# Kernel optimization log

Measured on AMD Instinct MI355X. Metric: run time of the kernel, lower is better.

Reference implementation:

```python
import jax, jax.numpy as jnp
import numpy as np

N = 50000   # nodes
E = 800000  # edges
R = 8       # relations
B = 4       # bases
NEG = 0.2   # leaky relu slope


def setup_inputs() -> dict:
    key = jax.random.key(0)
    ks = jax.random.split(key, 20)
    s = 0.1
    rn = lambda k, sh: jax.random.normal(k, sh, dtype=jnp.float32) * s
    return {
        "x": jax.random.normal(ks[0], (N, 64), dtype=jnp.float32),
        "edge_index": jax.random.randint(ks[1], (2, E), 0, N),
        "edge_type": jax.random.randint(ks[2], (E,), 0, R),
        # RGCN layer 1 (64 -> 64), basis decomposition
        "basis1": rn(ks[3], (B, 64, 64)), "comp1": rn(ks[4], (R, B)),
        "root1": rn(ks[5], (64, 64)), "brg1": jnp.zeros((64,), jnp.float32),
        # GAT layer 1 (64 -> 32, heads=4, concat -> 128)
        "wg1": rn(ks[6], (64, 128)), "asrc1": rn(ks[7], (4, 32)),
        "adst1": rn(ks[8], (4, 32)), "bg1": jnp.zeros((128,), jnp.float32),
        # RGCN layer 2 (128 -> 32)
        "basis2": rn(ks[9], (B, 128, 32)), "comp2": rn(ks[10], (R, B)),
        "root2": rn(ks[11], (128, 32)), "brg2": jnp.zeros((32,), jnp.float32),
        # GAT layer 2 (32 -> 16, heads=4, concat=False -> mean)
        "wg2": rn(ks[12], (32, 64)), "asrc2": rn(ks[13], (4, 16)),
        "adst2": rn(ks[14], (4, 16)), "bg2": jnp.zeros((16,), jnp.float32),
    }


def rgcn(x, src, dst, etype, basis, comp, root, bias):
    """PyG RGCNConv with basis decomposition, aggr='mean' per relation."""
    n, f = x.shape
    weight = jnp.einsum('rb,bio->rio', comp, basis)          # [R, in, out]
    seg = dst * R + etype                                    # per (node, relation) segment
    msg = x[src]                                             # [E, in] gather
    sums = jax.ops.segment_sum(msg, seg, num_segments=n * R).reshape(n, R, f)
    cnt = jax.ops.segment_sum(jnp.ones((src.shape[0],), x.dtype), seg,
                              num_segments=n * R).reshape(n, R, 1)
    mean = sums / jnp.maximum(cnt, 1.0)                      # [N, R, in]
    return jnp.einsum('nri,rio->no', mean, weight) + x @ root + bias


def gat(x, src, dst, w, a_src, a_dst, bias, heads, out_ch, concat):
    """PyG GATConv: add self loops, edge softmax over incoming edges."""
    n = x.shape[0]
    loop = jnp.arange(n)
    s2 = jnp.concatenate([src, loop])
    d2 = jnp.concatenate([dst, loop])
    h = (x @ w).reshape(n, heads, out_ch)                    # [N, H, C]
    al_src = (h * a_src).sum(-1)                             # [N, H]
    al_dst = (h * a_dst).sum(-1)                             # [N, H]
    e = jax.nn.leaky_relu(al_src[s2] + al_dst[d2], NEG)      # [E2, H]
    m = jax.ops.segment_max(e, d2, num_segments=n)           # stable softmax per dst
    e = jnp.exp(e - m[d2])
    z = jax.ops.segment_sum(e, d2, num_segments=n)
    alpha = e / z[d2]                                        # [E2, H]
    msg = h[s2] * alpha[:, :, None]                          # [E2, H, C]
    out = jax.ops.segment_sum(msg, d2, num_segments=n)       # [N, H, C]
    out = out.reshape(n, heads * out_ch) if concat else out.mean(axis=1)
    return out + bias


def reference(x, edge_index, edge_type,
              basis1, comp1, root1, brg1, wg1, asrc1, adst1, bg1,
              basis2, comp2, root2, brg2, wg2, asrc2, adst2, bg2):
    src, dst = edge_index[0], edge_index[1]
    # i=0: RGCN + relu (dropout p=0)
    x = jax.nn.relu(rgcn(x, src, dst, edge_type, basis1, comp1, root1, brg1))
    # i=1 == 2*pairs-1: GAT concat, NO activation
    x = gat(x, src, dst, wg1, asrc1, adst1, bg1, heads=4, out_ch=32, concat=True)
    # i=2: RGCN + relu
    x = jax.nn.relu(rgcn(x, src, dst, edge_type, basis2, comp2, root2, brg2))
    # i=3: GAT mean-heads + relu
    x = jax.nn.relu(gat(x, src, dst, wg2, asrc2, adst2, bg2, heads=4, out_ch=16, concat=False))
    return jnp.tanh(x)
```

## Files before the change

### kernel.cpp

```cpp
#include <hip/hip_runtime.h>
#include <math.h>

#define NN 50000
#define EE 800000
#define RR 8
#define SLOPE 0.2f
#define SEGS (NN * RR)
#define NBLK ((SEGS + 255) / 256)
#define NTW ((NN + 63) / 64)
#define NBUK 98
#define SEGB 4096
#define EB4 ((EE + 4095) / 4096)

typedef __attribute__((ext_vector_type(8))) short bf16x8;
typedef __attribute__((ext_vector_type(4))) float f32x4;
typedef _Float16 f16;
typedef __attribute__((ext_vector_type(4))) _Float16 h4;
typedef __attribute__((ext_vector_type(8))) _Float16 h8;

__device__ __forceinline__ float leaky(float v) { return v >= 0.f ? v : SLOPE * v; }

__device__ __forceinline__ void fmacc(float4& a, const float4& v, float p) {
    a.x = fmaf(v.x, p, a.x);
    a.y = fmaf(v.y, p, a.y);
    a.z = fmaf(v.z, p, a.z);
    a.w = fmaf(v.w, p, a.w);
}

__device__ __forceinline__ void red4(float4& a, int m) {
    a.x += __shfl_xor(a.x, m);
    a.y += __shfl_xor(a.y, m);
    a.z += __shfl_xor(a.z, m);
    a.w += __shfl_xor(a.w, m);
}

__device__ __forceinline__ float4 h4tof4(h4 t) {
    return make_float4((float)t.x, (float)t.y, (float)t.z, (float)t.w);
}

__device__ __forceinline__ void split8(const float4& v0, const float4& v1,
                                       bf16x8& hi, bf16x8& lo) {
    float e[8] = {v0.x, v0.y, v0.z, v0.w, v1.x, v1.y, v1.z, v1.w};
    union { bf16x8 v; unsigned u[4]; } H, L;
#pragma unroll
    for (int j = 0; j < 4; j++) {
        unsigned b0 = __float_as_uint(e[2 * j]), b1 = __float_as_uint(e[2 * j + 1]);
        unsigned h0 = b0 & 0xFFFF0000u, h1 = b1 & 0xFFFF0000u;
        H.u[j] = (h0 >> 16) | h1;
        float l0 = e[2 * j] - __uint_as_float(h0);
        float l1 = e[2 * j + 1] - __uint_as_float(h1);
        L.u[j] = (__float_as_uint(l0) >> 16) | (__float_as_uint(l1) & 0xFFFF0000u);
    }
    hi = H.v;
    lo = L.v;
}

__global__ void k_count2(const int* __restrict__ dst, const int* __restrict__ et,
                         int* __restrict__ cnt2) {
    int e = blockIdx.x * 256 + threadIdx.x;
    if (e < EE) atomicAdd(&cnt2[dst[e] * RR + et[e]], 1);
}

__global__ void k_scanA(const int* __restrict__ cnt2, int* __restrict__ rp,
                        int* __restrict__ bsum) {
    __shared__ int sh[256];
    int t = threadIdx.x;
    int i = blockIdx.x * 256 + t;
    int v = (i < SEGS) ? cnt2[i] : 0;
    sh[t] = v;
    __syncthreads();
    for (int off = 1; off < 256; off <<= 1) {
        int u = (t >= off) ? sh[t - off] : 0;
        __syncthreads();
        sh[t] += u;
        __syncthreads();
    }
    if (i < SEGS) rp[i] = sh[t] - v;
    if (t == 255) bsum[blockIdx.x] = sh[255];
}

__global__ void k_scanB(int* __restrict__ bsum) {
    __shared__ int sh[256];
    int t = threadIdx.x;
    int loc[8];
    int s = 0;
#pragma unroll
    for (int i = 0; i < 8; i++) {
        int idx = t * 8 + i;
        int v = (idx < NBLK) ? bsum[idx] : 0;
        loc[i] = v;
        s += v;
    }
    sh[t] = s;
    __syncthreads();
    for (int off = 1; off < 256; off <<= 1) {
        int u = (t >= off) ? sh[t - off] : 0;
        __syncthreads();
        sh[t] += u;
        __syncthreads();
    }
    int run = sh[t] - s;
#pragma unroll
    for (int i = 0; i < 8; i++) {
        int idx = t * 8 + i;
        if (idx < NBLK) {
            int v = loc[i];
            bsum[idx] = run;
            run += v;
        }
    }
}

__global__ void k_scanC(int* __restrict__ rp, const int* __restrict__ bsum) {
    int i = blockIdx.x * 256 + threadIdx.x;
    if (i < SEGS) rp[i] += bsum[blockIdx.x];
    if (i == 0) rp[SEGS] = EE;
}

__global__ void k_initcb(const int* __restrict__ rp, int* __restrict__ cbcur) {
    int t = threadIdx.x;
    if (t < NBUK) cbcur[t] = rp[t * SEGB];
}

__global__ __launch_bounds__(256) void k_fillA(const int* __restrict__ src,
                                               const int* __restrict__ dst,
                                               const int* __restrict__ et,
                                               int* __restrict__ cbcur,
                                               int* __restrict__ recbuf) {
    __shared__ int hist[NBUK], lcur[NBUK], gres[NBUK];
    int tid = threadIdx.x;
    int e0 = blockIdx.x * 4096;
    int cnt = EE - e0;
    if (cnt > 4096) cnt = 4096;
    for (int i = tid; i < NBUK; i += 256) { hist[i] = 0; lcur[i] = 0; }
    __syncthreads();
    int myb[16], myrec[16];
#pragma unroll
    for (int j = 0; j < 16; j++) {
        int i = tid + j * 256;
        if (i < cnt) {
            int e = e0 + i;
            int d = dst[e];
            int b = d >> 9;
            myb[j] = b;
            myrec[j] = ((d & 511) << 19) | (src[e] << 3) | et[e];
            atomicAdd(&hist[b], 1);
        } else {
            myb[j] = -1;
            myrec[j] = 0;
        }
    }
    __syncthreads();
    if (tid < NBUK) gres[tid] = atomicAdd(&cbcur[tid], hist[tid]);
    __syncthreads();
#pragma unroll
    for (int j = 0; j < 16; j++) {
        if (myb[j] >= 0) {
            int p = atomicAdd(&lcur[myb[j]], 1);
            recbuf[gres[myb[j]] + p] = myrec[j];
        }
    }
}

__global__ __launch_bounds__(256) void k_fillB(const int* __restrict__ rp,
                                               const int* __restrict__ recbuf,
                                               int* __restrict__ srcs2) {
    __shared__ int cur[SEGB];
    int b = blockIdx.x;
    int segbase = b * SEGB;
    int nseg = SEGS - segbase;
    if (nseg > SEGB) nseg = SEGB;
    int base = rp[segbase];
    int tid = threadIdx.x;
    for (int s = tid; s < SEGB; s += 256)
        cur[s] = (s < nseg) ? (rp[segbase + s] - base) : 0;
    __syncthreads();
    int limit = rp[segbase + nseg];
    int cnt = limit - base;
    for (int i = tid; i < cnt; i += 256) {
        int rec = recbuf[base + i];
        int segl = ((rec >> 19) << 3) | (rec & 7);
        int p = atomicAdd(&cur[segl], 1);
        srcs2[base + p] = rec & 0x7FFFF;
    }
}

__global__ void k_prep(const float* __restrict__ wg1, const float* __restrict__ wg2,
                       const float* __restrict__ root1, const float* __restrict__ root2,
                       const float* __restrict__ basis1, const float* __restrict__ basis2,
                       const float* __restrict__ comp2,
                       const float* __restrict__ asrc1, const float* __restrict__ adst1,
                       const float* __restrict__ asrc2, const float* __restrict__ adst2,
                       float* __restrict__ Wcat2e, float* __restrict__ wg1r,
                       float* __restrict__ Wstk, float* __restrict__ U1p,
                       float* __restrict__ U2p, float* __restrict__ Wb1) {
    int idx = blockIdx.x * 256 + threadIdx.x;
    if (idx < 16384) {
        int h = idx >> 12, kc = idx & 4095;
        int k = kc >> 6, c = kc & 63;
        wg1r[idx] = (c < 32) ? wg1[k * 128 + h * 32 + c] : 0.f;
    } else if (idx < 24576) {
        int j = idx - 16384;
        int row = j >> 6, c = j & 63;
        int h = row >> 5, k = row & 31;
        Wstk[j] = (c < 16) ? wg2[k * 64 + h * 16 + c] : 0.f;
    } else if (idx < 32768) {
        int j = idx - 24576;
        int k = j >> 6, c = j & 63;
        Wcat2e[k * 320 + c] = (c < 32) ? root2[k * 32 + c] : 0.f;
    } else if (idx < 36864) {
        int j0 = idx - 32768;
        int k = j0 >> 6, j = j0 & 63;
        float s = 0.f;
        if (j < 8) {
            int h = j & 3;
            const float* a = (j < 4) ? asrc1 : adst1;
            for (int c = 0; c < 32; c++) s += wg1[k * 128 + h * 32 + c] * a[h * 32 + c];
        }
        U1p[j0] = s;
    } else if (idx < 38912) {
        int j0 = idx - 36864;
        int k = j0 >> 6, j = j0 & 63;
        float s = 0.f;
        if (j < 8) {
            int h = j & 3;
            const float* a = (j < 4) ? asrc2 : adst2;
            for (int c = 0; c < 16; c++) s += wg2[k * 64 + h * 16 + c] * a[h * 16 + c];
        }
        U2p[j0] = s;
    } else if (idx < 55296) {
        Wb1[idx - 38912] = basis1[idx - 38912];
    } else if (idx < 59392) {
        Wb1[idx - 38912] = root1[idx - 55296];
    } else if (idx < 92160) {
        int j = idx - 59392;
        int i = j >> 8, rc = j & 255;
        int r = rc >> 5, o = rc & 31;
        float acc = 0.f;
#pragma unroll
        for (int b = 0; b < 4; b++) acc += comp2[r * 4 + b] * basis2[b * 4096 + i * 32 + o];
        Wcat2e[i * 320 + 64 + rc] = acc;
    }
}

__global__ void k_pack(const float* __restrict__ Wb1, const float* __restrict__ wg1r,
                       const float* __restrict__ Wcat, short* __restrict__ pWb1,
                       short* __restrict__ pwg1r, short* __restrict__ pWcat) {
    int u = blockIdx.x * 256 + threadIdx.x;
    int lane = u & 63, pair = u >> 6;
    if (pair >= 136) return;
    int m = lane & 15, g = lane >> 4;
    const float* src;
    int ldB, col, k0;
    short* dst;
    if (pair < 40) {
        int ct = pair / 10, kc = pair % 10;
        src = Wb1; ldB = 64; col = ct * 16 + m; k0 = kc * 32 + g * 8;
        dst = pWb1 + pair * 1024 + lane * 8;
    } else if (pair < 56) {
        int q = pair - 40;
        int h = q >> 2, lp = q & 3, ct = lp >> 1, kc = lp & 1;
        src = wg1r + h * 4096; ldB = 64; col = ct * 16 + m; k0 = kc * 32 + g * 8;
        dst = pwg1r + q * 1024 + lane * 8;
    } else {
        int q = pair - 56;
        int p = q >> 4, lp = q & 15, ct = lp >> 2, kc = lp & 3;
        src = Wcat; ldB = 320; col = p * 64 + ct * 16 + m; k0 = kc * 32 + g * 8;
        dst = pWcat + q * 1024 + lane * 8;
    }
    float e[8];
#pragma unroll
    for (int r = 0; r < 8; r++) e[r] = src[(size_t)(k0 + r) * ldB + col];
    union { bf16x8 v; unsigned u4[4]; } H, L;
#pragma unroll
    for (int j = 0; j < 4; j++) {
        unsigned b0 = __float_as_uint(e[2 * j]), b1 = __float_as_uint(e[2 * j + 1]);
        unsigned h0 = b0 & 0xFFFF0000u, h1 = b1 & 0xFFFF0000u;
        H.u4[j] = (h0 >> 16) | h1;
        float l0 = e[2 * j] - __uint_as_float(h0);
        float l1 = e[2 * j + 1] - __uint_as_float(h1);
        L.u4[j] = (__float_as_uint(l0) >> 16) | (__float_as_uint(l1) & 0xFFFF0000u);
    }
    *(bf16x8*)dst = H.v;
    *(bf16x8*)(dst + 512) = L.v;
}

template <int KTOT, int NCOL, int ACT = 0, int OUTH = 0>
__global__ __launch_bounds__(256) void k_mfma(const float* __restrict__ X, int ldX, int xmb,
                                              const short* __restrict__ Bpk, int bmb,
                                              float* __restrict__ Y, int ldY, size_t ymb,
                                              const float* __restrict__ bias, int biasmb) {
    constexpr int NKC = KTOT / 32;
    constexpr int NCT = NCOL / 16;
    const int tid = threadIdx.x;
    const int wid = tid >> 6, lane = tid & 63;
    const int m = lane & 15, g = lane >> 4;
    const int mb = blockIdx.y;
    const int rowbase = blockIdx.x * 64 + wid * 16;
    if (rowbase >= NN) return;
    const float* Xm = X + (size_t)mb * xmb + (size_t)(rowbase + m) * ldX;
    const short* Bm = Bpk + (size_t)mb * bmb;

    f32x4 acc[NCT];
#pragma unroll
    for (int c = 0; c < NCT; c++) acc[c] = (f32x4){0.f, 0.f, 0.f, 0.f};

#pragma unroll
    for (int kc = 0; kc < NKC; kc++) {
        float4 v0 = *(const float4*)(Xm + kc * 32 + g * 8);
        float4 v1 = *(const float4*)(Xm + kc * 32 + g * 8 + 4);
        bf16x8 ah, al;
        split8(v0, v1, ah, al);
#pragma unroll
        for (int ct = 0; ct < NCT; ct++) {
            const short* bp = Bm + (size_t)(ct * NKC + kc) * 1024 + lane * 8;
            bf16x8 bh = *(const bf16x8*)bp;
            bf16x8 bl = *(const bf16x8*)(bp + 512);
            acc[ct] = __builtin_amdgcn_mfma_f32_16x16x32_bf16(ah, bh, acc[ct], 0, 0, 0);
            acc[ct] = __builtin_amdgcn_mfma_f32_16x16x32_bf16(al, bh, acc[ct], 0, 0, 0);
            acc[ct] = __builtin_amdgcn_mfma_f32_16x16x32_bf16(ah, bl, acc[ct], 0, 0, 0);
        }
    }

#pragma unroll
    for (int ct = 0; ct < NCT; ct++) {
        int col = ct * 16 + m;
        float bv = bias ? bias[mb * biasmb + col] : 0.f;
#pragma unroll
        for (int i = 0; i < 4; i++) {
            float o = acc[ct][i] + bv;
            if (ACT == 2) o = fmaxf(o, 0.f);
            if (OUTH) {
                f16* Yh = (f16*)Y;
                Yh[(size_t)mb * ymb + (size_t)(rowbase + g * 4 + i) * ldY + col] = (f16)o;
            } else {
                Y[(size_t)mb * ymb + (size_t)(rowbase + g * 4 + i) * ldY + col] = o;
            }
        }
    }
}

__global__ __launch_bounds__(256) void k_gagg1(const int* __restrict__ rp,
                                               const int* __restrict__ srcs2,
                                               const float* __restrict__ comp,
                                               const float* __restrict__ X,
                                               float* __restrict__ U) {
    __shared__ float4 sh_w[4][8];
    int wid = threadIdx.x >> 6, lane = threadIdx.x & 63;
    int n = blockIdx.x * 4 + wid;
    int rpv = (lane <= 8) ? rp[n * RR + lane] : 0;
    int nxt = __shfl(rpv, (lane + 1) & 63);
    if (lane < 8) {
        float inv = 1.f / (float)((nxt - rpv) > 0 ? (nxt - rpv) : 1);
        float4 c = *(const float4*)(comp + lane * 4);
        sh_w[wid][lane] = make_float4(c.x * inv, c.y * inv, c.z * inv, c.w * inv);
    }
    int q = lane & 15;
    int beg = rp[n * RR], end = rp[n * RR + RR];
    float4 a0 = make_float4(0.f, 0.f, 0.f, 0.f);
    float4 a1 = a0, a2 = a0, a3 = a0;
    int k = beg + (lane >> 4);
    for (; k + 4 < end; k += 8) {
        int key0 = srcs2[k], key1 = srcs2[k + 4];
        float4 w0 = sh_w[wid][key0 & 7], w1 = sh_w[wid][key1 & 7];
        float4 v0 = *(const float4*)(X + (size_t)(key0 >> 3) * 64 + q * 4);
        float4 v1 = *(const float4*)(X + (size_t)(key1 >> 3) * 64 + q * 4);
        fmacc(a0, v0, w0.x);
        fmacc(a1, v0, w0.y);
        fmacc(a2, v0, w0.z);
        fmacc(a3, v0, w0.w);
        fmacc(a0, v1, w1.x);
        fmacc(a1, v1, w1.y);
        fmacc(a2, v1, w1.z);
        fmacc(a3, v1, w1.w);
    }
    if (k < end) {
        int key0 = srcs2[k];
        float4 w0 = sh_w[wid][key0 & 7];
        float4 v0 = *(const float4*)(X + (size_t)(key0 >> 3) * 64 + q * 4);
        fmacc(a0, v0, w0.x);
        fmacc(a1, v0, w0.y);
        fmacc(a2, v0, w0.z);
        fmacc(a3, v0, w0.w);
    }
    red4(a0, 16); red4(a0, 32);
    red4(a1, 16); red4(a1, 32);
    red4(a2, 16); red4(a2, 32);
    red4(a3, 16); red4(a3, 32);
    if (lane < 16) {
        float* un = U + (size_t)n * 320;
        *(float4*)(un + 0 * 64 + q * 4) = a0;
        *(float4*)(un + 1 * 64 + q * 4) = a1;
        *(float4*)(un + 2 * 64 + q * 4) = a2;
        *(float4*)(un + 3 * 64 + q * 4) = a3;
        *(float4*)(un + 256 + q * 4) = *(const float4*)(X + (size_t)n * 64 + q * 4);
    }
}

__global__ __launch_bounds__(256) void k_alds1(const float* __restrict__ X,
                                               const float* __restrict__ U1p,
                                               float* __restrict__ alds,
                                               f16* __restrict__ x1h) {
    __shared__ float sUT[8 * 68];
    int tid = threadIdx.x;
    for (int i = tid; i < 512; i += 256) {
        int j = i >> 6, c = i & 63;
        sUT[j * 68 + c] = U1p[c * 64 + j];
    }
    __syncthreads();
    int lane = tid & 63, wid = tid >> 6;
    int n = blockIdx.x * 32 + wid * 8 + (lane >> 3);
    int q = lane & 7;
    float x[8];
    if (n < NN) {
        float4 v0 = *(const float4*)(X + (size_t)n * 64 + q * 8);
        float4 v1 = *(const float4*)(X + (size_t)n * 64 + q * 8 + 4);
        x[0] = v0.x; x[1] = v0.y; x[2] = v0.z; x[3] = v0.w;
        x[4] = v1.x; x[5] = v1.y; x[6] = v1.z; x[7] = v1.w;
        h8 hv;
#pragma unroll
        for (int c = 0; c < 8; c++) hv[c] = (f16)x[c];
        *(h8*)(x1h + (size_t)n * 64 + q * 8) = hv;
    } else {
#pragma unroll
        for (int c = 0; c < 8; c++) x[c] = 0.f;
    }
    float al[8];
#pragma unroll
    for (int j = 0; j < 8; j++) {
        const float* u = &sUT[j * 68 + q * 8];
        float s = 0.f;
#pragma unroll
        for (int c = 0; c < 8; c++) s += x[c] * u[c];
        al[j] = s;
    }
#pragma unroll
    for (int m = 1; m < 8; m <<= 1)
#pragma unroll
        for (int j = 0; j < 8; j++) al[j] += __shfl_xor(al[j], m);
    if (n < NN) alds[(size_t)n * 8 + q] = al[q];
}

__global__ __launch_bounds__(256) void k_final(const float* __restrict__ Xm,
                                               const float* __restrict__ Wstk,
                                               const float* __restrict__ bg2,
                                               float* __restrict__ out) {
    __shared__ float sWT[16 * 132];
    int tid = threadIdx.x;
    for (int i = tid; i < 2048; i += 256) {
        int c = i >> 7, k = i & 127;
        sWT[c * 132 + k] = Wstk[k * 64 + c];
    }
    __syncthreads();
    int lane = tid & 63, wid = tid >> 6;
    int n = blockIdx.x * 32 + wid * 8 + (lane >> 3);
    int q = lane & 7;
    float x[16];
    if (n < NN) {
#pragma unroll
        for (int t = 0; t < 4; t++) {
            float4 v = *(const float4*)(Xm + (size_t)n * 128 + t * 32 + q * 4);
            x[t * 4 + 0] = v.x; x[t * 4 + 1] = v.y; x[t * 4 + 2] = v.z; x[t * 4 + 3] = v.w;
        }
    } else {
#pragma unroll
        for (int k = 0; k < 16; k++) x[k] = 0.f;
    }
    float al[16];
#pragma unroll
    for (int c = 0; c < 16; c++) {
        float s = 0.f;
#pragma unroll
        for (int t = 0; t < 4; t++) {
            const float* w = &sWT[c * 132 + t * 32 + q * 4];
            s += x[t * 4 + 0] * w[0] + x[t * 4 + 1] * w[1] + x[t * 4 + 2] * w[2] +
                 x[t * 4 + 3] * w[3];
        }
        al[c] = s;
    }
#pragma unroll
    for (int m = 1; m < 8; m <<= 1)
#pragma unroll
        for (int c = 0; c < 16; c++) al[c] += __shfl_xor(al[c], m);
    if (n < NN && q < 4) {
        float4 bv = *(const float4*)(bg2 + q * 4);
        float4 v;
        v.x = tanhf(fmaxf(0.25f * al[q * 4 + 0] + bv.x, 0.f));
        v.y = tanhf(fmaxf(0.25f * al[q * 4 + 1] + bv.y, 0.f));
        v.z = tanhf(fmaxf(0.25f * al[q * 4 + 2] + bv.z, 0.f));
        v.w = tanhf(fmaxf(0.25f * al[q * 4 + 3] + bv.w, 0.f));
        *(float4*)(out + (size_t)n * 16 + q * 4) = v;
    }
}

__global__ __launch_bounds__(256) void k_agg2(const int* __restrict__ rp,
                                              const int* __restrict__ srcs2,
                                              const f16* __restrict__ y,
                                              const float* __restrict__ bias,
                                              const float* __restrict__ U2p,
                                              const float* __restrict__ x3prev,
                                              f16* __restrict__ x3h,
                                              float* __restrict__ alds) {
    __shared__ float sh_inv[4][8];
    int wid = threadIdx.x >> 6, lane = threadIdx.x & 63;
    int n = blockIdx.x * 4 + wid;
    int rpv = (lane <= 8) ? rp[n * RR + lane] : 0;
    int nxt = __shfl(rpv, (lane + 1) & 63);
    if (lane < 8) sh_inv[wid][lane] = 1.f / (float)((nxt - rpv) > 0 ? (nxt - rpv) : 1);
    int q = lane & 7;
    int beg = rp[n * RR], end = rp[n * RR + RR];
    float4 acc = make_float4(0.f, 0.f, 0.f, 0.f);
    int k = beg + (lane >> 3);
    for (; k + 8 < end; k += 16) {
        int key0 = srcs2[k], key1 = srcs2[k + 8];
        int s0 = key0 >> 3, s1 = key1 >> 3;
        int g0 = key0 & 7, g1 = key1 & 7;
        float e0 = sh_inv[wid][g0], e1 = sh_inv[wid][g1];
        float4 v0 = h4tof4(*(const h4*)(y + ((size_t)(g0 >> 1) * NN + s0) * 64 + (g0 & 1) * 32 + q * 4));
        float4 v1 = h4tof4(*(const h4*)(y + ((size_t)(g1 >> 1) * NN + s1) * 64 + (g1 & 1) * 32 + q * 4));
        fmacc(acc, v0, e0);
        fmacc(acc, v1, e1);
    }
    if (k < end) {
        int key0 = srcs2[k];
        int s0 = key0 >> 3;
        int g0 = key0 & 7;
        float4 v0 = h4tof4(*(const h4*)(y + ((size_t)(g0 >> 1) * NN + s0) * 64 + (g0 & 1) * 32 + q * 4));
        fmacc(acc, v0, sh_inv[wid][g0]);
    }
    red4(acc, 8);
    red4(acc, 16);
    red4(acc, 32);
    if (lane < 8) {
        float4 prev = *(const float4*)(x3prev + (size_t)n * 64 + q * 4);
        float4 b = *(const float4*)(bias + q * 4);
        float4 v;
        v.x = fmaxf(prev.x + acc.x + b.x, 0.f);
        v.y = fmaxf(prev.y + acc.y + b.y, 0.f);
        v.z = fmaxf(prev.z + acc.z + b.z, 0.f);
        v.w = fmaxf(prev.w + acc.w + b.w, 0.f);
        h4 hv = {(f16)v.x, (f16)v.y, (f16)v.z, (f16)v.w};
        *(h4*)(x3h + (size_t)n * 32 + q * 4) = hv;
        float al[8];
#pragma unroll
        for (int j = 0; j < 8; j++) {
            al[j] = fmaf(v.x, U2p[(q * 4 + 0) * 64 + j],
                    fmaf(v.y, U2p[(q * 4 + 1) * 64 + j],
                    fmaf(v.z, U2p[(q * 4 + 2) * 64 + j],
                         v.w * U2p[(q * 4 + 3) * 64 + j])));
        }
#pragma unroll
        for (int m = 1; m < 8; m <<= 1) {
#pragma unroll
            for (int j = 0; j < 8; j++) al[j] += __shfl_xor(al[j], m);
        }
        alds[n * 8 + q] = al[q];
    }
}

template <int F, int LDX = F>
__global__ __launch_bounds__(256) void k_gatx(const int* __restrict__ rp,
                                              const int* __restrict__ srcs2,
                                              const float* __restrict__ alds,
                                              const f16* __restrict__ X,
                                              float* __restrict__ msg) {
    constexpr int G = F / 4;
    constexpr int NG = 64 / G;
    int wid = threadIdx.x >> 6, lane = threadIdx.x & 63;
    int n = blockIdx.x * 4 + wid;
    if (n >= NN) return;
    int g = lane / G, q = lane % G;
    float4 ald4 = *(const float4*)(alds + n * 8 + 4);
    float4 acc0 = make_float4(0.f, 0.f, 0.f, 0.f);
    float4 acc1 = acc0, acc2 = acc0, acc3 = acc0;
    float4 z = make_float4(0.f, 0.f, 0.f, 0.f);
    if (g == 0) {
        float4 a4 = *(const float4*)(alds + n * 8);
        float4 xv = h4tof4(*(const h4*)(X + (size_t)n * LDX + q * 4));
        float p0 = __expf(leaky(a4.x + ald4.x));
        float p1 = __expf(leaky(a4.y + ald4.y));
        float p2 = __expf(leaky(a4.z + ald4.z));
        float p3 = __expf(leaky(a4.w + ald4.w));
        z = make_float4(p0, p1, p2, p3);
        fmacc(acc0, xv, p0);
        fmacc(acc1, xv, p1);
        fmacc(acc2, xv, p2);
        fmacc(acc3, xv, p3);
    }
    int beg = rp[n * RR], end = rp[n * RR + RR];
    int k = beg + g;
    for (; k + NG < end; k += 2 * NG) {
        int s0 = srcs2[k] >> 3, s1 = srcs2[k + NG] >> 3;
        float4 a0 = *(const float4*)(alds + s0 * 8);
        float4 a1 = *(const float4*)(alds + s1 * 8);
        float4 x0 = h4tof4(*(const h4*)(X + (size_t)s0 * LDX + q * 4));
        float4 x1v = h4tof4(*(const h4*)(X + (size_t)s1 * LDX + q * 4));
        float p00 = __expf(leaky(a0.x + ald4.x)), p01 = __expf(leaky(a0.y + ald4.y));
        float p02 = __expf(leaky(a0.z + ald4.z)), p03 = __expf(leaky(a0.w + ald4.w));
        float p10 = __expf(leaky(a1.x + ald4.x)), p11 = __expf(leaky(a1.y + ald4.y));
        float p12 = __expf(leaky(a1.z + ald4.z)), p13 = __expf(leaky(a1.w + ald4.w));
        z.x += p00 + p10;
        z.y += p01 + p11;
        z.z += p02 + p12;
        z.w += p03 + p13;
        fmacc(acc0, x0, p00);
        fmacc(acc1, x0, p01);
        fmacc(acc2, x0, p02);
        fmacc(acc3, x0, p03);
        fmacc(acc0, x1v, p10);
        fmacc(acc1, x1v, p11);
        fmacc(acc2, x1v, p12);
        fmacc(acc3, x1v, p13);
    }
    if (k < end) {
        int s0 = srcs2[k] >> 3;
        float4 a0 = *(const float4*)(alds + s0 * 8);
        float4 x0 = h4tof4(*(const h4*)(X + (size_t)s0 * LDX + q * 4));
        float p00 = __expf(leaky(a0.x + ald4.x)), p01 = __expf(leaky(a0.y + ald4.y));
        float p02 = __expf(leaky(a0.z + ald4.z)), p03 = __expf(leaky(a0.w + ald4.w));
        z.x += p00;
        z.y += p01;
        z.z += p02;
        z.w += p03;
        fmacc(acc0, x0, p00);
        fmacc(acc1, x0, p01);
        fmacc(acc2, x0, p02);
        fmacc(acc3, x0, p03);
    }
#pragma unroll
    for (int m = G; m < 64; m <<= 1) {
        red4(acc0, m);
        red4(acc1, m);
        red4(acc2, m);
        red4(acc3, m);
        red4(z, m);
    }
    if (g == 0) {
        float4 iz = make_float4(1.f / z.x, 1.f / z.y, 1.f / z.z, 1.f / z.w);
        float* mp = msg + (size_t)n * 4 * F + q * 4;
        *(float4*)(mp + 0 * F) = make_float4(acc0.x * iz.x, acc0.y * iz.x, acc0.z * iz.x, acc0.w * iz.x);
        *(float4*)(mp + 1 * F) = make_float4(acc1.x * iz.y, acc1.y * iz.y, acc1.z * iz.y, acc1.w * iz.y);
        *(float4*)(mp + 2 * F) = make_float4(acc2.x * iz.z, acc2.y * iz.z, acc2.z * iz.z, acc2.w * iz.z);
        *(float4*)(mp + 3 * F) = make_float4(acc3.x * iz.w, acc3.y * iz.w, acc3.z * iz.w, acc3.w * iz.w);
    }
}

extern "C" void kernel_launch(void* const* d_in, const int* in_sizes, int n_in,
                              void* d_out, int out_size, void* d_ws, size_t ws_size,
                              hipStream_t stream) {
    const float* x      = (const float*)d_in[0];
    const int*   ei     = (const int*)d_in[1];
    const int*   et     = (const int*)d_in[2];
    const float* basis1 = (const float*)d_in[3];
    const float* comp1  = (const float*)d_in[4];
    const float* root1  = (const float*)d_in[5];
    const float* brg1   = (const float*)d_in[6];
    const float* wg1    = (const float*)d_in[7];
    const float* asrc1  = (const float*)d_in[8];
    const float* adst1  = (const float*)d_in[9];
    const float* bg1    = (const float*)d_in[10];
    const float* basis2 = (const float*)d_in[11];
    const float* comp2  = (const float*)d_in[12];
    const float* root2  = (const float*)d_in[13];
    const float* brg2   = (const float*)d_in[14];
    const float* wg2    = (const float*)d_in[15];
    const float* asrc2  = (const float*)d_in[16];
    const float* adst2  = (const float*)d_in[17];
    const float* bg2    = (const float*)d_in[18];
    const int* src = ei;
    const int* dst = ei + EE;
    float* out = (float*)d_out;

    int* wsi = (int*)d_ws;
    size_t ioff = 0;
    auto ialloc = [&](size_t n) { int* p = wsi + ioff; ioff += (n + 3) & ~(size_t)3; return p; };
    int* cnt2 = ialloc(SEGS);
    int* rp   = ialloc(SEGS + 1);
    int* bsum = ialloc(2048);
    int* srcs2 = ialloc(EE);
    int* recbuf = ialloc(EE);
    int* cbcur = ialloc(128);
    float* wsf = (float*)(wsi + ioff);
    size_t total_f = (ws_size - ioff * sizeof(int)) / sizeof(float);
    size_t P_f = (size_t)NN * 320;
    size_t need_f = P_f + (size_t)NN * 128
                  + 40960 + 20480 + 16384 + 8192 + 4096 + 2048
                  + (size_t)NN * 8
                  + 20480 + 8192 + 40960
                  + (size_t)NN * 32 + (size_t)NN * 16 + 64;
    if (total_f < need_f) return;
    size_t foff = 0;
    auto falloc = [&](size_t n) { float* p = wsf + foff; foff += (n + 3) & ~(size_t)3; return p; };
    float* P      = falloc(P_f);
    float* x2     = falloc((size_t)NN * 128);
    float* Wcat2e = falloc(40960);
    float* Wb1    = falloc(20480);
    float* wg1r   = falloc(16384);
    float* Wstk   = falloc(8192);
    float* U1p    = falloc(4096);
    float* U2p    = falloc(2048);
    float* alds   = falloc((size_t)NN * 8);
    short* Wb1pk  = (short*)falloc(20480);
    short* wg1rpk = (short*)falloc(8192);
    short* Wcatpk = (short*)falloc(40960);
    f16* x1h      = (f16*)falloc((size_t)NN * 32);
    f16* x3h      = (f16*)falloc((size_t)NN * 16);
    float* Ubuf = P;
    float* x1   = x2 + (size_t)NN * 64;
    float* msg1 = P;
    float* x3   = P;
    f16* ybuf3h = (f16*)(P + (size_t)NN * 64);
    float* msg2 = P + (size_t)NN * 64;

    const int EB = (EE + 255) / 256;
    const int NB4 = (NN + 3) / 4;
    const int NB32 = (NN + 31) / 32;

    hipMemsetAsync(cnt2, 0, SEGS * sizeof(int), stream);
    k_count2<<<EB, 256, 0, stream>>>(dst, et, cnt2);
    k_scanA<<<NBLK, 256, 0, stream>>>(cnt2, rp, bsum);
    k_scanB<<<1, 256, 0, stream>>>(bsum);
    k_scanC<<<NBLK, 256, 0, stream>>>(rp, bsum);
    k_initcb<<<1, 128, 0, stream>>>(rp, cbcur);
    k_fillA<<<EB4, 256, 0, stream>>>(src, dst, et, cbcur, recbuf);
    k_fillB<<<NBUK, 256, 0, stream>>>(rp, recbuf, srcs2);
    k_prep<<<(92160 + 255) / 256, 256, 0, stream>>>(
        wg1, wg2, root1, root2, basis1, basis2, comp2, asrc1, adst1, asrc2, adst2,
        Wcat2e, wg1r, Wstk, U1p, U2p, Wb1);
    k_pack<<<34, 256, 0, stream>>>(Wb1, wg1r, Wcat2e, Wb1pk, wg1rpk, Wcatpk);

    k_gagg1<<<NB4, 256, 0, stream>>>(rp, srcs2, comp1, x, Ubuf);
    k_mfma<320, 64, 2><<<dim3(NTW, 1), 256, 0, stream>>>(Ubuf, 320, 0, Wb1pk, 0,
                                                         x1, 64, 0, brg1, 0);

    k_alds1<<<NB32, 256, 0, stream>>>(x1, U1p, alds, x1h);
    k_gatx<64, 64><<<NB4, 256, 0, stream>>>(rp, srcs2, alds, x1h, msg1);
    k_mfma<64, 32, 0><<<dim3(NTW, 4), 256, 0, stream>>>(msg1, 256, 64, wg1rpk, 4096,
                                                        x2, 128, 32, bg1, 32);

    k_mfma<128, 64, 0, 0><<<dim3(NTW, 1), 256, 0, stream>>>(x2, 128, 0, Wcatpk, 0,
                                                            P, 64, 0, nullptr, 0);
    k_mfma<128, 64, 0, 1><<<dim3(NTW, 4), 256, 0, stream>>>(x2, 128, 0, Wcatpk + 16384, 16384,
                                                            (float*)ybuf3h, 64, (size_t)NN * 64,
                                                            nullptr, 0);
    k_agg2<<<NB4, 256, 0, stream>>>(rp, srcs2, ybuf3h, brg2, U2p, x3, x3h, alds);

    k_gatx<32, 32><<<NB4, 256, 0, stream>>>(rp, srcs2, alds, x3h, msg2);
    k_final<<<NB32, 256, 0, stream>>>(msg2, Wstk, bg2, out);
}
```

Baseline: 441.2 us.

## Precompute per-node exp factors for GAT softmax and store messages in fp16

```diff
diff --git a/kernel.cpp b/kernel.cpp
--- a/kernel.cpp
+++ b/kernel.cpp
@@ -285,7 +285,7 @@
     *(bf16x8*)(dst + 512) = L.v;
 }
 
-template <int KTOT, int NCOL, int ACT = 0, int OUTH = 0>
+template <int KTOT, int NCOL, int ACT = 0, int OUTH = 0, int AH = 0>
 __global__ __launch_bounds__(256) void k_mfma(const float* __restrict__ X, int ldX, int xmb,
                                               const short* __restrict__ Bpk, int bmb,
                                               float* __restrict__ Y, int ldY, size_t ymb,
@@ -299,6 +299,7 @@
     const int rowbase = blockIdx.x * 64 + wid * 16;
     if (rowbase >= NN) return;
     const float* Xm = X + (size_t)mb * xmb + (size_t)(rowbase + m) * ldX;
+    const f16* Xmh = (const f16*)X + (size_t)mb * xmb + (size_t)(rowbase + m) * ldX;
     const short* Bm = Bpk + (size_t)mb * bmb;
 
     f32x4 acc[NCT];
@@ -307,8 +308,15 @@
 
 #pragma unroll
     for (int kc = 0; kc < NKC; kc++) {
-        float4 v0 = *(const float4*)(Xm + kc * 32 + g * 8);
-        float4 v1 = *(const float4*)(Xm + kc * 32 + g * 8 + 4);
+        float4 v0, v1;
+        if (AH) {
+            h8 hv = *(const h8*)(Xmh + kc * 32 + g * 8);
+            v0 = make_float4((float)hv[0], (float)hv[1], (float)hv[2], (float)hv[3]);
+            v1 = make_float4((float)hv[4], (float)hv[5], (float)hv[6], (float)hv[7]);
+        } else {
+            v0 = *(const float4*)(Xm + kc * 32 + g * 8);
+            v1 = *(const float4*)(Xm + kc * 32 + g * 8 + 4);
+        }
         bf16x8 ah, al;
         split8(v0, v1, ah, al);
 #pragma unroll
@@ -399,7 +407,7 @@
 
 __global__ __launch_bounds__(256) void k_alds1(const float* __restrict__ X,
                                                const float* __restrict__ U1p,
-                                               float* __restrict__ alds,
+                                               float* __restrict__ aldsE,
                                                f16* __restrict__ x1h) {
     __shared__ float sUT[8 * 68];
     int tid = threadIdx.x;
@@ -438,10 +446,15 @@
     for (int m = 1; m < 8; m <<= 1)
 #pragma unroll
         for (int j = 0; j < 8; j++) al[j] += __shfl_xor(al[j], m);
-    if (n < NN) alds[(size_t)n * 8 + q] = al[q];
-}
-
-__global__ __launch_bounds__(256) void k_final(const float* __restrict__ Xm,
+    if (n < NN) {
+        float av = al[q];
+        int pos = (q < 4) ? q : q + 4;
+        aldsE[(size_t)n * 16 + pos] = __expf(av);
+        aldsE[(size_t)n * 16 + pos + 4] = __expf(SLOPE * av);
+    }
+}
+
+__global__ __launch_bounds__(256) void k_final(const f16* __restrict__ Xm,
                                                const float* __restrict__ Wstk,
                                                const float* __restrict__ bg2,
                                                float* __restrict__ out) {
@@ -459,7 +472,7 @@
     if (n < NN) {
 #pragma unroll
         for (int t = 0; t < 4; t++) {
-            float4 v = *(const float4*)(Xm + (size_t)n * 128 + t * 32 + q * 4);
+            float4 v = h4tof4(*(const h4*)(Xm + (size_t)n * 128 + t * 32 + q * 4));
             x[t * 4 + 0] = v.x; x[t * 4 + 1] = v.y; x[t * 4 + 2] = v.z; x[t * 4 + 3] = v.w;
         }
     } else {
@@ -500,7 +513,7 @@
                                               const float* __restrict__ U2p,
                                               const float* __restrict__ x3prev,
                                               f16* __restrict__ x3h,
-                                              float* __restrict__ alds) {
+                                              float* __restrict__ aldsE) {
     __shared__ float sh_inv[4][8];
     int wid = threadIdx.x >> 6, lane = threadIdx.x & 63;
     int n = blockIdx.x * 4 + wid;
@@ -554,33 +567,38 @@
 #pragma unroll
             for (int j = 0; j < 8; j++) al[j] += __shfl_xor(al[j], m);
         }
-        alds[n * 8 + q] = al[q];
+        float av = al[q];
+        int pos = (q < 4) ? q : q + 4;
+        aldsE[(size_t)n * 16 + pos] = __expf(av);
+        aldsE[(size_t)n * 16 + pos + 4] = __expf(SLOPE * av);
     }
 }
 
 template <int F, int LDX = F>
 __global__ __launch_bounds__(256) void k_gatx(const int* __restrict__ rp,
                                               const int* __restrict__ srcs2,
-                                              const float* __restrict__ alds,
+                                              const float* __restrict__ aldsE,
                                               const f16* __restrict__ X,
-                                              float* __restrict__ msg) {
+                                              f16* __restrict__ msg) {
     constexpr int G = F / 4;
     constexpr int NG = 64 / G;
     int wid = threadIdx.x >> 6, lane = threadIdx.x & 63;
     int n = blockIdx.x * 4 + wid;
     if (n >= NN) return;
     int g = lane / G, q = lane % G;
-    float4 ald4 = *(const float4*)(alds + n * 8 + 4);
+    float4 Ed = *(const float4*)(aldsE + (size_t)n * 16 + 8);
+    float4 Ed2 = *(const float4*)(aldsE + (size_t)n * 16 + 12);
     float4 acc0 = make_float4(0.f, 0.f, 0.f, 0.f);
     float4 acc1 = acc0, acc2 = acc0, acc3 = acc0;
     float4 z = make_float4(0.f, 0.f, 0.f, 0.f);
     if (g == 0) {
-        float4 a4 = *(const float4*)(alds + n * 8);
+        float4 Es = *(const float4*)(aldsE + (size_t)n * 16);
+        float4 Es2 = *(const float4*)(aldsE + (size_t)n * 16 + 4);
         float4 xv = h4tof4(*(const h4*)(X + (size_t)n * LDX + q * 4));
-        float p0 = __expf(leaky(a4.x + ald4.x));
-        float p1 = __expf(leaky(a4.y + ald4.y));
-        float p2 = __expf(leaky(a4.z + ald4.z));
-        float p3 = __expf(leaky(a4.w + ald4.w));
+        float p0 = fmaxf(Es.x * Ed.x, Es2.x * Ed2.x);
+        float p1 = fmaxf(Es.y * Ed.y, Es2.y * Ed2.y);
+        float p2 = fmaxf(Es.z * Ed.z, Es2.z * Ed2.z);
+        float p3 = fmaxf(Es.w * Ed.w, Es2.w * Ed2.w);
         z = make_float4(p0, p1, p2, p3);
         fmacc(acc0, xv, p0);
         fmacc(acc1, xv, p1);
@@ -591,14 +609,16 @@
     int k = beg + g;
     for (; k + NG < end; k += 2 * NG) {
         int s0 = srcs2[k] >> 3, s1 = srcs2[k + NG] >> 3;
-        float4 a0 = *(const float4*)(alds + s0 * 8);
-        float4 a1 = *(const float4*)(alds + s1 * 8);
+        float4 a0 = *(const float4*)(aldsE + (size_t)s0 * 16);
+        float4 b0 = *(const float4*)(aldsE + (size_t)s0 * 16 + 4);
+        float4 a1 = *(const float4*)(aldsE + (size_t)s1 * 16);
+        float4 b1 = *(const float4*)(aldsE + (size_t)s1 * 16 + 4);
         float4 x0 = h4tof4(*(const h4*)(X + (size_t)s0 * LDX + q * 4));
         float4 x1v = h4tof4(*(const h4*)(X + (size_t)s1 * LDX + q * 4));
-        float p00 = __expf(leaky(a0.x + ald4.x)), p01 = __expf(leaky(a0.y + ald4.y));
-        float p02 = __expf(leaky(a0.z + ald4.z)), p03 = __expf(leaky(a0.w + ald4.w));
-        float p10 = __expf(leaky(a1.x + ald4.x)), p11 = __expf(leaky(a1.y + ald4.y));
-        float p12 = __expf(leaky(a1.z + ald4.z)), p13 = __expf(leaky(a1.w + ald4.w));
+        float p00 = fmaxf(a0.x * Ed.x, b0.x * Ed2.x), p01 = fmaxf(a0.y * Ed.y, b0.y * Ed2.y);
+        float p02 = fmaxf(a0.z * Ed.z, b0.z * Ed2.z), p03 = fmaxf(a0.w * Ed.w, b0.w * Ed2.w);
+        float p10 = fmaxf(a1.x * Ed.x, b1.x * Ed2.x), p11 = fmaxf(a1.y * Ed.y, b1.y * Ed2.y);
+        float p12 = fmaxf(a1.z * Ed.z, b1.z * Ed2.z), p13 = fmaxf(a1.w * Ed.w, b1.w * Ed2.w);
         z.x += p00 + p10;
         z.y += p01 + p11;
         z.z += p02 + p12;
@@ -614,10 +634,11 @@
     }
     if (k < end) {
         int s0 = srcs2[k] >> 3;
-        float4 a0 = *(const float4*)(alds + s0 * 8);
+        float4 a0 = *(const float4*)(aldsE + (size_t)s0 * 16);
+        float4 b0 = *(const float4*)(aldsE + (size_t)s0 * 16 + 4);
         float4 x0 = h4tof4(*(const h4*)(X + (size_t)s0 * LDX + q * 4));
-        float p00 = __expf(leaky(a0.x + ald4.x)), p01 = __expf(leaky(a0.y + ald4.y));
-        float p02 = __expf(leaky(a0.z + ald4.z)), p03 = __expf(leaky(a0.w + ald4.w));
+        float p00 = fmaxf(a0.x * Ed.x, b0.x * Ed2.x), p01 = fmaxf(a0.y * Ed.y, b0.y * Ed2.y);
+        float p02 = fmaxf(a0.z * Ed.z, b0.z * Ed2.z), p03 = fmaxf(a0.w * Ed.w, b0.w * Ed2.w);
         z.x += p00;
         z.y += p01;
         z.z += p02;
@@ -637,11 +658,15 @@
     }
     if (g == 0) {
         float4 iz = make_float4(1.f / z.x, 1.f / z.y, 1.f / z.z, 1.f / z.w);
-        float* mp = msg + (size_t)n * 4 * F + q * 4;
-        *(float4*)(mp + 0 * F) = make_float4(acc0.x * iz.x, acc0.y * iz.x, acc0.z * iz.x, acc0.w * iz.x);
-        *(float4*)(mp + 1 * F) = make_float4(acc1.x * iz.y, acc1.y * iz.y, acc1.z * iz.y, acc1.w * iz.y);
-        *(float4*)(mp + 2 * F) = make_float4(acc2.x * iz.z, acc2.y * iz.z, acc2.z * iz.z, acc2.w * iz.z);
-        *(float4*)(mp + 3 * F) = make_float4(acc3.x * iz.w, acc3.y * iz.w, acc3.z * iz.w, acc3.w * iz.w);
+        f16* mp = msg + (size_t)n * 4 * F + q * 4;
+        h4 o0 = {(f16)(acc0.x * iz.x), (f16)(acc0.y * iz.x), (f16)(acc0.z * iz.x), (f16)(acc0.w * iz.x)};
+        h4 o1 = {(f16)(acc1.x * iz.y), (f16)(acc1.y * iz.y), (f16)(acc1.z * iz.y), (f16)(acc1.w * iz.y)};
+        h4 o2 = {(f16)(acc2.x * iz.z), (f16)(acc2.y * iz.z), (f16)(acc2.z * iz.z), (f16)(acc2.w * iz.z)};
+        h4 o3 = {(f16)(acc3.x * iz.w), (f16)(acc3.y * iz.w), (f16)(acc3.z * iz.w), (f16)(acc3.w * iz.w)};
+        *(h4*)(mp + 0 * F) = o0;
+        *(h4*)(mp + 1 * F) = o1;
+        *(h4*)(mp + 2 * F) = o2;
+        *(h4*)(mp + 3 * F) = o3;
     }
 }
 
@@ -685,7 +710,7 @@
     size_t P_f = (size_t)NN * 320;
     size_t need_f = P_f + (size_t)NN * 128
                   + 40960 + 20480 + 16384 + 8192 + 4096 + 2048
-                  + (size_t)NN * 8
+                  + (size_t)NN * 16
                   + 20480 + 8192 + 40960
                   + (size_t)NN * 32 + (size_t)NN * 16 + 64;
     if (total_f < need_f) return;
@@ -699,7 +724,7 @@
     float* Wstk   = falloc(8192);
     float* U1p    = falloc(4096);
     float* U2p    = falloc(2048);
-    float* alds   = falloc((size_t)NN * 8);
+    float* aldsE  = falloc((size_t)NN * 16);
     short* Wb1pk  = (short*)falloc(20480);
     short* wg1rpk = (short*)falloc(8192);
     short* Wcatpk = (short*)falloc(40960);
@@ -707,10 +732,10 @@
     f16* x3h      = (f16*)falloc((size_t)NN * 16);
     float* Ubuf = P;
     float* x1   = x2 + (size_t)NN * 64;
-    float* msg1 = P;
+    f16* msg1h  = (f16*)P;
     float* x3   = P;
     f16* ybuf3h = (f16*)(P + (size_t)NN * 64);
-    float* msg2 = P + (size_t)NN * 64;
+    f16* msg2h  = (f16*)(P + (size_t)NN * 64);
 
     const int EB = (EE + 255) / 256;
     const int NB4 = (NN + 3) / 4;
@@ -733,18 +758,19 @@
     k_mfma<320, 64, 2><<<dim3(NTW, 1), 256, 0, stream>>>(Ubuf, 320, 0, Wb1pk, 0,
                                                          x1, 64, 0, brg1, 0);
 
-    k_alds1<<<NB32, 256, 0, stream>>>(x1, U1p, alds, x1h);
-    k_gatx<64, 64><<<NB4, 256, 0, stream>>>(rp, srcs2, alds, x1h, msg1);
-    k_mfma<64, 32, 0><<<dim3(NTW, 4), 256, 0, stream>>>(msg1, 256, 64, wg1rpk, 4096,
-                                                        x2, 128, 32, bg1, 32);
+    k_alds1<<<NB32, 256, 0, stream>>>(x1, U1p, aldsE, x1h);
+    k_gatx<64, 64><<<NB4, 256, 0, stream>>>(rp, srcs2, aldsE, x1h, msg1h);
+    k_mfma<64, 32, 0, 0, 1><<<dim3(NTW, 4), 256, 0, stream>>>((const float*)msg1h, 256, 64,
+                                                              wg1rpk, 4096,
+                                                              x2, 128, 32, bg1, 32);
 
     k_mfma<128, 64, 0, 0><<<dim3(NTW, 1), 256, 0, stream>>>(x2, 128, 0, Wcatpk, 0,
                                                             P, 64, 0, nullptr, 0);
     k_mfma<128, 64, 0, 1><<<dim3(NTW, 4), 256, 0, stream>>>(x2, 128, 0, Wcatpk + 16384, 16384,
                                                             (float*)ybuf3h, 64, (size_t)NN * 64,
                                                             nullptr, 0);
-    k_agg2<<<NB4, 256, 0, stream>>>(rp, srcs2, ybuf3h, brg2, U2p, x3, x3h, alds);
-
-    k_gatx<32, 32><<<NB4, 256, 0, stream>>>(rp, srcs2, alds, x3h, msg2);
-    k_final<<<NB32, 256, 0, stream>>>(msg2, Wstk, bg2, out);
-}
+    k_agg2<<<NB4, 256, 0, stream>>>(rp, srcs2, ybuf3h, brg2, U2p, x3, x3h, aldsE);
+
+    k_gatx<32, 32><<<NB4, 256, 0, stream>>>(rp, srcs2, aldsE, x3h, msg2h);
+    k_final<<<NB32, 256, 0, stream>>>(msg2h, Wstk, bg2, out);
+}
```

After: 445.7 us. About the same (+1.0%).
